# Kernel tuning notes

Hardware: AMD Instinct MI355X
Metric: run time of the kernel (lower is better)

The kernel has to match this reference:

```python
import jax, jax.numpy as jnp
import numpy as np

N, B, L = 1000, 16, 12
H, IN_DIM, OUT_DIM, E = 64, 3, 1, 16000


def _gru_cell(x, h, Wi, Wh, bi, bh):
    # torch nn.GRU gate order: r, z, n
    gi = x @ Wi.T + bi
    gh = h @ Wh.T + bh
    ir, iz, inn = jnp.split(gi, 3, axis=-1)
    hr, hz, hn = jnp.split(gh, 3, axis=-1)
    r = jax.nn.sigmoid(ir + hr)
    z = jax.nn.sigmoid(iz + hz)
    n = jnp.tanh(inn + r * hn)
    return (1.0 - z) * n + z * h


def setup_inputs():
    key = jax.random.key(0)
    ks = jax.random.split(key, 24)
    def rn(k, shape, s=0.1):
        return jax.random.normal(k, shape, dtype=jnp.float32) * s
    return {
        "hidden0": rn(ks[0], (N, B, H), 1.0),
        "hidden1": rn(ks[1], (N, B, H), 1.0),
        "features": rn(ks[2], (N, H), 1.0),
        "labels": rn(ks[3], (N, B, L, IN_DIM), 1.0),
        "edge_index": jax.random.randint(ks[4], (2, E), 0, N),
        # GRU1: input_dim -> H
        "Wi1": rn(ks[5], (3 * H, IN_DIM)), "Wh1": rn(ks[6], (3 * H, H)),
        "bi1": rn(ks[7], (3 * H,)), "bh1": rn(ks[8], (3 * H,)),
        # MetaGAT MLP: 2H -> 16 -> 2 -> 2H*H
        "W1": rn(ks[9], (16, 2 * H)), "b1": rn(ks[10], (16,)),
        "W2": rn(ks[11], (2, 16)), "b2": rn(ks[12], (2,)),
        "W3": rn(ks[13], (2 * H * H, 2)), "b3": rn(ks[14], (2 * H * H,)),
        # GRU2: H -> H
        "Wi2": rn(ks[15], (3 * H, H)), "Wh2": rn(ks[16], (3 * H, H)),
        "bi2": rn(ks[17], (3 * H,)), "bh2": rn(ks[18], (3 * H,)),
        # output layer: 2H -> OUT_DIM
        "Wo": rn(ks[19], (OUT_DIM, 2 * H)), "bo": rn(ks[20], (OUT_DIM,)),
    }


def reference(hidden0, hidden1, features, labels, edge_index,
              Wi1, Wh1, bi1, bh1, W1, b1, W2, b2, W3, b3,
              Wi2, Wh2, bi2, bh2, Wo, bo):
    n, b, length, _ = labels.shape
    h = Wh1.shape[1]
    out_dim = Wo.shape[0]
    in_dim = Wi1.shape[1]
    aux = labels[..., out_dim:]  # [N,B,L,aux_dim]
    # add self loops (as in MetaGAT.forward)
    loops = jnp.arange(n)
    src = jnp.concatenate([edge_index[0], loops])  # j, source
    dst = jnp.concatenate([edge_index[1], loops])  # i, target
    # per-edge weight matrices; features are constant across timesteps so hoist
    ft = jnp.concatenate([features[dst], features[src]], axis=-1)  # [Etot,2H]
    w = jax.nn.sigmoid(ft @ W1.T + b1)
    w = jax.nn.sigmoid(w @ W2.T + b2)
    w = (w @ W3.T + b3).reshape(-1, 2 * h, h)  # [Etot,2H,H]
    feat_b = jnp.broadcast_to(features[:, None, :], (n, b, features.shape[-1]))

    def step(carry, idx):
        h0, h1, prev = carry
        aux_prev = jnp.take(aux, jnp.maximum(idx - 1, 0), axis=2)  # [N,B,aux]
        # eval path (train_mode=False): feed back previous prediction
        data = jnp.where(idx == 0,
                         jnp.zeros((n, b, in_dim), labels.dtype),
                         jnp.concatenate([prev, aux_prev], axis=-1))
        h0n = _gru_cell(data.reshape(n * b, in_dim), h0.reshape(n * b, h),
                        Wi1, Wh1, bi1, bh1).reshape(n, b, h)
        # MetaGAT message passing
        st_j = h0n[src]                                  # [Etot,B,H]
        st = jnp.concatenate([h0n[dst], st_j], axis=-1)  # [Etot,B,2H]
        alpha = jax.nn.leaky_relu(jnp.einsum('ebk,ekh->ebh', st, w), 0.01)
        alpha = jax.nn.softmax(alpha, axis=1)            # softmax over batch dim (faithful to source)
        agg = jax.ops.segment_sum(alpha * st_j, dst, num_segments=n)
        gat = jax.nn.relu(agg)                           # [N,B,H]
        h1n = _gru_cell(gat.reshape(n * b, h), h1.reshape(n * b, h),
                        Wi2, Wh2, bi2, bh2).reshape(n, b, h)
        pred = jnp.concatenate([h1n, feat_b], axis=-1) @ Wo.T + bo  # [N,B,out_dim]
        return (h0n, h1n, pred), pred

    init = (hidden0, hidden1, jnp.zeros((n, b, out_dim), labels.dtype))
    _, preds = jax.lax.scan(step, init, jnp.arange(length))
    return jnp.moveaxis(preds, 0, 2)  # [N,B,L,out_dim]
```

## Files before the change

kernel.cpp:

```cpp
#include <hip/hip_runtime.h>

#define N_NODES 1000
#define BATCH 16
#define SEQ 12
#define IN_DIM 3
#define HDIM 64
#define E_EDGES 16000
#define EN (E_EDGES + N_NODES)
#define NB (N_NODES * BATCH)

typedef unsigned int u32;
typedef unsigned short u16;

__device__ __forceinline__ float sigmoidf(float x) { return 1.0f / (1.0f + expf(-x)); }

__device__ __forceinline__ u16 f2bf(float x) {
    u32 u = __builtin_bit_cast(u32, x);
    u32 r = (u + 0x7fffu + ((u >> 16) & 1u)) >> 16;
    return (u16)r;
}
__device__ __forceinline__ float bf2f(u32 h) {
    return __builtin_bit_cast(float, (h & 0xffffu) << 16);
}
__device__ __forceinline__ u32 pack2(float a, float b) {
    return (u32)f2bf(a) | ((u32)f2bf(b) << 16);
}

__global__ void prep_kernel(const float* __restrict__ hidden0,
                            const float* __restrict__ hidden1,
                            const float* __restrict__ features,
                            const float* __restrict__ W3,
                            const float* __restrict__ b3,
                            const float* __restrict__ Wo,
                            const float* __restrict__ bo,
                            const float* __restrict__ Wh1,
                            const float* __restrict__ Wi1,
                            const float* __restrict__ Wi2,
                            const float* __restrict__ Wh2,
                            float* __restrict__ h0, float* __restrict__ h1,
                            float* __restrict__ M,
                            float* __restrict__ Wh1T, float* __restrict__ Wi1T,
                            float* __restrict__ Wi2T, float* __restrict__ Wh2T,
                            float* __restrict__ fpred, float* __restrict__ prev)
{
    int tid = blockIdx.x * blockDim.x + threadIdx.x;
    int stride = gridDim.x * blockDim.x;

    for (int i = tid; i < NB * HDIM; i += stride) { h0[i] = hidden0[i]; h1[i] = hidden1[i]; }

    for (int i = tid; i < 64 * 384; i += stride) {
        int k = i / 384, c = i % 384;
        int grp = c / 64, h = c % 64;
        int kk = (grp < 3 ? k : 64 + k) * 64 + h;
        float val;
        if (grp == 0 || grp == 3)      val = W3[kk * 2 + 0];
        else if (grp == 1 || grp == 4) val = W3[kk * 2 + 1];
        else                           val = b3[kk];
        M[i] = val;
    }

    for (int i = tid; i < 192 * 64; i += stride) {
        int k = i / 192, gj = i % 192;
        Wh1T[i] = Wh1[gj * 64 + k];
        Wi2T[i] = Wi2[gj * 64 + k];
        Wh2T[i] = Wh2[gj * 64 + k];
    }
    for (int i = tid; i < 3 * 192; i += stride) {
        int c = i / 192, gj = i % 192;
        Wi1T[i] = Wi1[gj * 3 + c];
    }

    for (int i = tid; i < NB; i += stride) prev[i] = 0.0f;

    for (int n = tid; n < N_NODES; n += stride) {
        float acc = bo[0];
        for (int h = 0; h < HDIM; ++h) acc += features[n * HDIM + h] * Wo[64 + h];
        fpred[n] = acc;
    }
}

__global__ void deg_init_kernel(int* __restrict__ deg)
{
    int n = blockIdx.x * blockDim.x + threadIdx.x;
    if (n < N_NODES) deg[n] = 1;
}

__global__ void deg_count_kernel(const int* __restrict__ edge_index, int* __restrict__ deg)
{
    int e = blockIdx.x * blockDim.x + threadIdx.x;
    if (e < E_EDGES) atomicAdd(&deg[edge_index[E_EDGES + e]], 1);
}

__global__ __launch_bounds__(1024) void scan_kernel(const int* __restrict__ deg,
                                                    int* __restrict__ row_ptr,
                                                    int* __restrict__ row_fill)
{
    __shared__ int s[1024];
    int tid = threadIdx.x;
    int x = (tid < N_NODES) ? deg[tid] : 0;
    s[tid] = x;
    __syncthreads();
    for (int off = 1; off < 1024; off <<= 1) {
        int v = (tid >= off) ? s[tid - off] : 0;
        __syncthreads();
        s[tid] += v;
        __syncthreads();
    }
    int incl = s[tid];
    int excl = incl - x;
    if (tid < N_NODES) { row_ptr[tid] = excl; row_fill[tid] = excl; }
    if (tid == N_NODES - 1) row_ptr[N_NODES] = incl;
}

__global__ void scatter_kernel(const int* __restrict__ edge_index,
                               int* __restrict__ row_fill,
                               int* __restrict__ csr_src,
                               int* __restrict__ perm)
{
    int e = blockIdx.x * blockDim.x + threadIdx.x;
    if (e < E_EDGES) {
        int s = edge_index[e];
        int d = edge_index[E_EDGES + e];
        int p = atomicAdd(&row_fill[d], 1);
        csr_src[p] = s;
        perm[e] = p;
    } else if (e < EN) {
        int n = e - E_EDGES;
        int p = atomicAdd(&row_fill[n], 1);
        csr_src[p] = n;
        perm[e] = p;
    }
}

__global__ __launch_bounds__(256) void edge_mlp_kernel(const int* __restrict__ edge_index,
                                                       const float* __restrict__ features,
                                                       const float* __restrict__ W1,
                                                       const float* __restrict__ b1,
                                                       const float* __restrict__ W2,
                                                       const float* __restrict__ b2,
                                                       const int* __restrict__ perm,
                                                       float* __restrict__ csr_uv)
{
    int w = threadIdx.x >> 6, j = threadIdx.x & 63;
    int e = blockIdx.x * 4 + w;
    int s, d;
    if (e < E_EDGES) { s = edge_index[e]; d = edge_index[E_EDGES + e]; }
    else             { s = e - E_EDGES; d = s; }

    __shared__ float ft[4][128];
    __shared__ float w1s[4][16];
    ft[w][j]      = features[d * HDIM + j];
    ft[w][64 + j] = features[s * HDIM + j];
    __syncthreads();

    int o = j & 15, part = j >> 4;
    float acc = 0.0f;
    #pragma unroll 8
    for (int kk = 0; kk < 32; ++kk)
        acc += ft[w][part * 32 + kk] * W1[o * 128 + part * 32 + kk];
    acc += __shfl_xor(acc, 16, 64);
    acc += __shfl_xor(acc, 32, 64);
    if (j < 16) w1s[w][j] = sigmoidf(acc + b1[j]);
    __syncthreads();
    if (j < 2) {
        float a2 = b2[j];
        #pragma unroll
        for (int k = 0; k < 16; ++k) a2 += w1s[w][k] * W2[j * 16 + k];
        csr_uv[perm[e] * 2 + j] = sigmoidf(a2);
    }
}

__global__ __launch_bounds__(256) void gru1_proj_kernel(const float* __restrict__ labels,
                                                        const float* __restrict__ prev,
                                                        const float* __restrict__ Wi1T,
                                                        const float* __restrict__ Wh1T,
                                                        const float* __restrict__ bi1,
                                                        const float* __restrict__ bh1,
                                                        const float* __restrict__ M,
                                                        float* __restrict__ h0,
                                                        uint2* __restrict__ Pd,
                                                        uint2* __restrict__ Ps,
                                                        int t)
{
    int w = threadIdx.x >> 6, j = threadIdx.x & 63;
    int rbase = blockIdx.x * 32 + w * 8;
    __shared__ float hs[32][64];

    #pragma unroll
    for (int rr = 0; rr < 8; ++rr)
        hs[w * 8 + rr][j] = h0[(size_t)(rbase + rr) * HDIM + j];

    float ar[8], az[8], an[8];
    {
        float br = bh1[j], bz = bh1[64 + j], bn = bh1[128 + j];
        #pragma unroll
        for (int rr = 0; rr < 8; ++rr) { ar[rr] = br; az[rr] = bz; an[rr] = bn; }
    }

    for (int k = 0; k < 64; k += 2) {
        const float* w0 = &Wh1T[(size_t)k * 192 + j];
        float wr0 = w0[0], wz0 = w0[64], wn0 = w0[128];
        float wr1 = w0[192], wz1 = w0[256], wn1 = w0[320];
        #pragma unroll
        for (int rr = 0; rr < 8; ++rr) {
            float2 h2 = *(const float2*)&hs[w * 8 + rr][k];
            ar[rr] = fmaf(wr0, h2.x, ar[rr]);
            az[rr] = fmaf(wz0, h2.x, az[rr]);
            an[rr] = fmaf(wn0, h2.x, an[rr]);
            ar[rr] = fmaf(wr1, h2.y, ar[rr]);
            az[rr] = fmaf(wz1, h2.y, az[rr]);
            an[rr] = fmaf(wn1, h2.y, an[rr]);
        }
    }

    float wi00 = Wi1T[j],       wi01 = Wi1T[64 + j],       wi02 = Wi1T[128 + j];
    float wi10 = Wi1T[192 + j], wi11 = Wi1T[192 + 64 + j], wi12 = Wi1T[192 + 128 + j];
    float wi20 = Wi1T[384 + j], wi21 = Wi1T[384 + 64 + j], wi22 = Wi1T[384 + 128 + j];
    float bir = bi1[j], biz = bi1[64 + j], bin_ = bi1[128 + j];

    #pragma unroll
    for (int rr = 0; rr < 8; ++rr) {
        int row = rbase + rr;
        float x0 = 0.f, x1 = 0.f, x2 = 0.f;
        if (t > 0) {
            x0 = prev[row];
            const float* lab = labels + ((size_t)row * SEQ + (t - 1)) * IN_DIM;
            x1 = lab[1]; x2 = lab[2];
        }
        float gir = bir  + x0 * wi00 + x1 * wi10 + x2 * wi20;
        float giz = biz  + x0 * wi01 + x1 * wi11 + x2 * wi21;
        float gin = bin_ + x0 * wi02 + x1 * wi12 + x2 * wi22;
        float rg = sigmoidf(gir + ar[rr]);
        float zg = sigmoidf(giz + az[rr]);
        float ng = tanhf(gin + rg * an[rr]);
        float hj = hs[w * 8 + rr][j];
        float hn = (1.0f - zg) * ng + zg * hj;
        h0[(size_t)row * HDIM + j] = hn;
        hs[w * 8 + rr][j] = hn;
    }

    float a0[8], a1[8], a2[8], a3[8], a4[8], a5[8];
    #pragma unroll
    for (int rr = 0; rr < 8; ++rr) { a0[rr]=0.f; a1[rr]=0.f; a2[rr]=0.f; a3[rr]=0.f; a4[rr]=0.f; a5[rr]=0.f; }

    for (int k = 0; k < 64; ++k) {
        const float* mrow = &M[(size_t)k * 384 + j];
        float m0 = mrow[0],   m1 = mrow[64],  m2 = mrow[128];
        float m3 = mrow[192], m4 = mrow[256], m5 = mrow[320];
        #pragma unroll
        for (int rr = 0; rr < 8; ++rr) {
            float hk = hs[w * 8 + rr][k];
            a0[rr] = fmaf(m0, hk, a0[rr]); a1[rr] = fmaf(m1, hk, a1[rr]);
            a2[rr] = fmaf(m2, hk, a2[rr]); a3[rr] = fmaf(m3, hk, a3[rr]);
            a4[rr] = fmaf(m4, hk, a4[rr]); a5[rr] = fmaf(m5, hk, a5[rr]);
        }
    }

    #pragma unroll
    for (int rr = 0; rr < 8; ++rr) {
        size_t row = rbase + rr;
        float stj = hs[w * 8 + rr][j];
        Pd[row * 64 + j] = make_uint2(pack2(a0[rr], a1[rr]), pack2(a2[rr], 0.f));
        Ps[row * 64 + j] = make_uint2(pack2(a3[rr], a4[rr]), pack2(a5[rr], stj));
    }
}

__global__ __launch_bounds__(256) void edge_step_kernel(const int* __restrict__ row_ptr,
                                                        const int* __restrict__ csr_src,
                                                        const float* __restrict__ csr_uv,
                                                        const uint2* __restrict__ Pd,
                                                        const uint2* __restrict__ Ps,
                                                        float* __restrict__ agg)
{
    int d = blockIdx.x;
    int w = threadIdx.x >> 6, h = threadIdx.x & 63;

    uint2 pdreg[BATCH];
    #pragma unroll
    for (int b = 0; b < BATCH; ++b)
        pdreg[b] = Pd[((size_t)d * BATCH + b) * 64 + h];

    float acc[BATCH];
    #pragma unroll
    for (int b = 0; b < BATCH; ++b) acc[b] = 0.0f;

    int start = row_ptr[d], end = row_ptr[d + 1];
    for (int p = start + w; p < end; p += 4) {
        int s = csr_src[p];
        float u = csr_uv[p * 2], v = csr_uv[p * 2 + 1];

        float al[BATCH], stj[BATCH];
        #pragma unroll
        for (int b = 0; b < BATCH; ++b) {
            uint2 pd = pdreg[b];
            uint2 ps = Ps[((size_t)s * BATCH + b) * 64 + h];
            float c0 = bf2f(pd.x), c1 = bf2f(pd.x >> 16), c2 = bf2f(pd.y);
            float c3 = bf2f(ps.x), c4 = bf2f(ps.x >> 16), c5 = bf2f(ps.y);
            float a = u * (c0 + c3) + v * (c1 + c4) + c2 + c5;
            al[b] = (a > 0.0f) ? a : 0.01f * a;
            stj[b] = bf2f(ps.y >> 16);
        }
        float m = al[0];
        #pragma unroll
        for (int b = 1; b < BATCH; ++b) m = fmaxf(m, al[b]);
        float sum = 0.0f;
        #pragma unroll
        for (int b = 0; b < BATCH; ++b) { al[b] = expf(al[b] - m); sum += al[b]; }
        float inv = 1.0f / sum;
        #pragma unroll
        for (int b = 0; b < BATCH; ++b) acc[b] = fmaf(al[b] * inv, stj[b], acc[b]);
    }

    __shared__ float red[4][BATCH][HDIM];
    #pragma unroll
    for (int b = 0; b < BATCH; ++b) red[w][b][h] = acc[b];
    __syncthreads();

    for (int c = threadIdx.x; c < BATCH * HDIM; c += 256) {
        float s4 = red[0][0][c] + red[1][0][c] + red[2][0][c] + red[3][0][c];
        agg[(size_t)d * BATCH * HDIM + c] = s4;
    }
}

__global__ __launch_bounds__(256) void gru2_pred_kernel(const float* __restrict__ agg,
                                                        const float* __restrict__ Wi2T,
                                                        const float* __restrict__ Wh2T,
                                                        const float* __restrict__ bi2,
                                                        const float* __restrict__ bh2,
                                                        const float* __restrict__ Wo,
                                                        const float* __restrict__ fpred,
                                                        float* __restrict__ h1,
                                                        float* __restrict__ prev,
                                                        float* __restrict__ out,
                                                        int t)
{
    int w = threadIdx.x >> 6, j = threadIdx.x & 63;
    int rbase = blockIdx.x * 32 + w * 8;
    __shared__ float gs[32][64];
    __shared__ float hs[32][64];

    #pragma unroll
    for (int rr = 0; rr < 8; ++rr) {
        float g = agg[(size_t)(rbase + rr) * HDIM + j];
        gs[w * 8 + rr][j] = fmaxf(g, 0.0f);
        hs[w * 8 + rr][j] = h1[(size_t)(rbase + rr) * HDIM + j];
    }

    float acr[8], acz[8], ain[8], ahn[8];
    {
        float b0 = bi2[j] + bh2[j], b1 = bi2[64 + j] + bh2[64 + j];
        float b2 = bi2[128 + j], c2 = bh2[128 + j];
        #pragma unroll
        for (int rr = 0; rr < 8; ++rr) { acr[rr] = b0; acz[rr] = b1; ain[rr] = b2; ahn[rr] = c2; }
    }

    for (int k = 0; k < 64; ++k) {
        const float* wiRow = &Wi2T[(size_t)k * 192 + j];
        const float* whRow = &Wh2T[(size_t)k * 192 + j];
        float wir = wiRow[0], wiz = wiRow[64], win = wiRow[128];
        float whr = whRow[0], whz = whRow[64], whn = whRow[128];
        #pragma unroll
        for (int rr = 0; rr < 8; ++rr) {
            float gk = gs[w * 8 + rr][k];
            float hk = hs[w * 8 + rr][k];
            acr[rr] = fmaf(wir, gk, acr[rr]);  acr[rr] = fmaf(whr, hk, acr[rr]);
            acz[rr] = fmaf(wiz, gk, acz[rr]);  acz[rr] = fmaf(whz, hk, acz[rr]);
            ain[rr] = fmaf(win, gk, ain[rr]);  ahn[rr] = fmaf(whn, hk, ahn[rr]);
        }
    }

    float woj = Wo[j];
    #pragma unroll
    for (int rr = 0; rr < 8; ++rr) {
        float rg = sigmoidf(acr[rr]);
        float zg = sigmoidf(acz[rr]);
        float ng = tanhf(ain[rr] + rg * ahn[rr]);
        float hj = hs[w * 8 + rr][j];
        float hn = (1.0f - zg) * ng + zg * hj;
        h1[(size_t)(rbase + rr) * HDIM + j] = hn;

        float part = hn * woj;
        #pragma unroll
        for (int off = 32; off; off >>= 1) part += __shfl_xor(part, off, 64);
        if (j == rr) {
            int row = rbase + rr;
            float p = part + fpred[row / BATCH];
            prev[row] = p;
            out[(size_t)row * SEQ + t] = p;
        }
    }
}

extern "C" void kernel_launch(void* const* d_in, const int* in_sizes, int n_in,
                              void* d_out, int out_size, void* d_ws, size_t ws_size,
                              hipStream_t stream)
{
    const float* hidden0  = (const float*)d_in[0];
    const float* hidden1  = (const float*)d_in[1];
    const float* features = (const float*)d_in[2];
    const float* labels   = (const float*)d_in[3];
    const int*   edge_idx = (const int*)d_in[4];
    const float* Wi1 = (const float*)d_in[5];
    const float* Wh1 = (const float*)d_in[6];
    const float* bi1 = (const float*)d_in[7];
    const float* bh1 = (const float*)d_in[8];
    const float* W1  = (const float*)d_in[9];
    const float* b1  = (const float*)d_in[10];
    const float* W2  = (const float*)d_in[11];
    const float* b2  = (const float*)d_in[12];
    const float* W3  = (const float*)d_in[13];
    const float* b3  = (const float*)d_in[14];
    const float* Wi2 = (const float*)d_in[15];
    const float* Wh2 = (const float*)d_in[16];
    const float* bi2 = (const float*)d_in[17];
    const float* bh2 = (const float*)d_in[18];
    const float* Wo  = (const float*)d_in[19];
    const float* bo  = (const float*)d_in[20];

    float* ws = (float*)d_ws;
    float* h0    = ws;  ws += NB * HDIM;
    float* h1    = ws;  ws += NB * HDIM;
    uint2* Pd    = (uint2*)ws;  ws += NB * HDIM * 2;
    uint2* Ps    = (uint2*)ws;  ws += NB * HDIM * 2;
    float* agg   = ws;  ws += NB * HDIM;
    float* csr_uv= ws;  ws += EN * 2;
    float* M     = ws;  ws += 64 * 384;
    float* Wh1T  = ws;  ws += 64 * 192;
    float* Wi1T  = ws;  ws += 3 * 192;
    float* Wi2T  = ws;  ws += 64 * 192;
    float* Wh2T  = ws;  ws += 64 * 192;
    float* fpred = ws;  ws += N_NODES;
    float* prev  = ws;  ws += NB;
    int*   deg      = (int*)ws;  ws += N_NODES;
    int*   row_ptr  = (int*)ws;  ws += N_NODES + 1;
    int*   row_fill = (int*)ws;  ws += N_NODES;
    int*   csr_src  = (int*)ws;  ws += EN;
    int*   perm     = (int*)ws;  ws += EN;
    float* out   = (float*)d_out;

    prep_kernel<<<256, 256, 0, stream>>>(hidden0, hidden1, features, W3, b3, Wo, bo,
                                         Wh1, Wi1, Wi2, Wh2,
                                         h0, h1, M, Wh1T, Wi1T, Wi2T, Wh2T, fpred, prev);
    deg_init_kernel<<<(N_NODES + 255) / 256, 256, 0, stream>>>(deg);
    deg_count_kernel<<<(E_EDGES + 255) / 256, 256, 0, stream>>>(edge_idx, deg);
    scan_kernel<<<1, 1024, 0, stream>>>(deg, row_ptr, row_fill);
    scatter_kernel<<<(EN + 255) / 256, 256, 0, stream>>>(edge_idx, row_fill, csr_src, perm);
    edge_mlp_kernel<<<(EN + 3) / 4, 256, 0, stream>>>(edge_idx, features, W1, b1, W2, b2,
                                                      perm, csr_uv);

    for (int t = 0; t < SEQ; ++t) {
        gru1_proj_kernel<<<NB / 32, 256, 0, stream>>>(labels, prev, Wi1T, Wh1T, bi1, bh1,
                                                      M, h0, Pd, Ps, t);
        edge_step_kernel<<<N_NODES, 256, 0, stream>>>(row_ptr, csr_src, csr_uv, Pd, Ps, agg);
        gru2_pred_kernel<<<NB / 32, 256, 0, stream>>>(agg, Wi2T, Wh2T, bi2, bh2, Wo, fpred,
                                                      h1, prev, out, t);
    }
}
```

Measured before the change: 993.9 us.

## Fuse edge aggregation, GRU2, prediction and next-step GRU1 into one per-node kernel

The per-timestep edge aggregation, GRU2 plus output prediction, and the next timestep's GRU1 plus projection are merged into a single kernel with one block per destination node. A separate t=0 GRU1 kernel runs before the loop. Ping-pong Pd/Ps buffers keep the reads of the current projections apart from the writes of the next ones. This drops the agg and prev global round trips and two launches per step, but the per-node blocks now handle only 16 rows each and run the GRU matmuls with 4 rows per wave instead of 8, which lowers weight reuse.

```diff
diff --git a/kernel.cpp b/kernel.cpp
--- a/kernel.cpp
+++ b/kernel.cpp
@@ -41,7 +41,7 @@
                             float* __restrict__ M,
                             float* __restrict__ Wh1T, float* __restrict__ Wi1T,
                             float* __restrict__ Wi2T, float* __restrict__ Wh2T,
-                            float* __restrict__ fpred, float* __restrict__ prev)
+                            float* __restrict__ fpred)
 {
     int tid = blockIdx.x * blockDim.x + threadIdx.x;
     int stride = gridDim.x * blockDim.x;
@@ -69,8 +69,6 @@
         int c = i / 192, gj = i % 192;
         Wi1T[i] = Wi1[gj * 3 + c];
     }
-
-    for (int i = tid; i < NB; i += stride) prev[i] = 0.0f;
 
     for (int n = tid; n < N_NODES; n += stride) {
         float acc = bo[0];
@@ -170,17 +168,13 @@
     }
 }
 
-__global__ __launch_bounds__(256) void gru1_proj_kernel(const float* __restrict__ labels,
-                                                        const float* __restrict__ prev,
-                                                        const float* __restrict__ Wi1T,
-                                                        const float* __restrict__ Wh1T,
-                                                        const float* __restrict__ bi1,
-                                                        const float* __restrict__ bh1,
-                                                        const float* __restrict__ M,
-                                                        float* __restrict__ h0,
-                                                        uint2* __restrict__ Pd,
-                                                        uint2* __restrict__ Ps,
-                                                        int t)
+__global__ __launch_bounds__(256) void gru1_proj_t0_kernel(const float* __restrict__ Wh1T,
+                                                           const float* __restrict__ bi1,
+                                                           const float* __restrict__ bh1,
+                                                           const float* __restrict__ M,
+                                                           float* __restrict__ h0,
+                                                           uint2* __restrict__ Pd,
+                                                           uint2* __restrict__ Ps)
 {
     int w = threadIdx.x >> 6, j = threadIdx.x & 63;
     int rbase = blockIdx.x * 32 + w * 8;
@@ -213,43 +207,238 @@
         }
     }
 
+    float bir = bi1[j], biz = bi1[64 + j], bin_ = bi1[128 + j];
+
+    #pragma unroll
+    for (int rr = 0; rr < 8; ++rr) {
+        float rg = sigmoidf(bir + ar[rr]);
+        float zg = sigmoidf(biz + az[rr]);
+        float ng = tanhf(bin_ + rg * an[rr]);
+        float hj = hs[w * 8 + rr][j];
+        float hn = (1.0f - zg) * ng + zg * hj;
+        h0[(size_t)(rbase + rr) * HDIM + j] = hn;
+        hs[w * 8 + rr][j] = hn;
+    }
+
+    float a0[8], a1[8], a2[8], a3[8], a4[8], a5[8];
+    #pragma unroll
+    for (int rr = 0; rr < 8; ++rr) { a0[rr]=0.f; a1[rr]=0.f; a2[rr]=0.f; a3[rr]=0.f; a4[rr]=0.f; a5[rr]=0.f; }
+
+    for (int k = 0; k < 64; ++k) {
+        const float* mrow = &M[(size_t)k * 384 + j];
+        float m0 = mrow[0],   m1 = mrow[64],  m2 = mrow[128];
+        float m3 = mrow[192], m4 = mrow[256], m5 = mrow[320];
+        #pragma unroll
+        for (int rr = 0; rr < 8; ++rr) {
+            float hk = hs[w * 8 + rr][k];
+            a0[rr] = fmaf(m0, hk, a0[rr]); a1[rr] = fmaf(m1, hk, a1[rr]);
+            a2[rr] = fmaf(m2, hk, a2[rr]); a3[rr] = fmaf(m3, hk, a3[rr]);
+            a4[rr] = fmaf(m4, hk, a4[rr]); a5[rr] = fmaf(m5, hk, a5[rr]);
+        }
+    }
+
+    #pragma unroll
+    for (int rr = 0; rr < 8; ++rr) {
+        size_t row = rbase + rr;
+        float stj = hs[w * 8 + rr][j];
+        Pd[row * 64 + j] = make_uint2(pack2(a0[rr], a1[rr]), pack2(a2[rr], 0.f));
+        Ps[row * 64 + j] = make_uint2(pack2(a3[rr], a4[rr]), pack2(a5[rr], stj));
+    }
+}
+
+__global__ __launch_bounds__(256) void step_kernel(const int* __restrict__ row_ptr,
+                                                   const int* __restrict__ csr_src,
+                                                   const float* __restrict__ csr_uv,
+                                                   const uint2* __restrict__ Pdr,
+                                                   const uint2* __restrict__ Psr,
+                                                   uint2* __restrict__ Pdw,
+                                                   uint2* __restrict__ Psw,
+                                                   const float* __restrict__ Wi2T,
+                                                   const float* __restrict__ Wh2T,
+                                                   const float* __restrict__ bi2,
+                                                   const float* __restrict__ bh2,
+                                                   const float* __restrict__ Wo,
+                                                   const float* __restrict__ fpred,
+                                                   float* __restrict__ h1,
+                                                   float* __restrict__ out,
+                                                   const float* __restrict__ labels,
+                                                   const float* __restrict__ Wi1T,
+                                                   const float* __restrict__ Wh1T,
+                                                   const float* __restrict__ bi1,
+                                                   const float* __restrict__ bh1,
+                                                   const float* __restrict__ M,
+                                                   float* __restrict__ h0,
+                                                   int t, int last)
+{
+    int d = blockIdx.x;
+    int w = threadIdx.x >> 6, j = threadIdx.x & 63;
+    int rbase = d * BATCH + w * 4;
+
+    __shared__ float red[4][BATCH][HDIM];
+    __shared__ float gs[BATCH][HDIM];
+    __shared__ float hs[BATCH][HDIM];
+    __shared__ float prevs[BATCH];
+
+    uint2 pdreg[BATCH];
+    #pragma unroll
+    for (int b = 0; b < BATCH; ++b)
+        pdreg[b] = Pdr[((size_t)d * BATCH + b) * 64 + j];
+
+    float acc[BATCH];
+    #pragma unroll
+    for (int b = 0; b < BATCH; ++b) acc[b] = 0.0f;
+
+    int start = row_ptr[d], end = row_ptr[d + 1];
+    for (int p = start + w; p < end; p += 4) {
+        int s = csr_src[p];
+        float u = csr_uv[p * 2], v = csr_uv[p * 2 + 1];
+
+        float al[BATCH], stj[BATCH];
+        #pragma unroll
+        for (int b = 0; b < BATCH; ++b) {
+            uint2 pd = pdreg[b];
+            uint2 ps = Psr[((size_t)s * BATCH + b) * 64 + j];
+            float a = u * (bf2f(pd.x) + bf2f(ps.x))
+                    + v * (bf2f(pd.x >> 16) + bf2f(ps.x >> 16))
+                    + bf2f(pd.y) + bf2f(ps.y);
+            al[b] = (a > 0.0f) ? a : 0.01f * a;
+            stj[b] = bf2f(ps.y >> 16);
+        }
+        float m = al[0];
+        #pragma unroll
+        for (int b = 1; b < BATCH; ++b) m = fmaxf(m, al[b]);
+        float sum = 0.0f;
+        #pragma unroll
+        for (int b = 0; b < BATCH; ++b) { al[b] = expf(al[b] - m); sum += al[b]; }
+        float inv = 1.0f / sum;
+        #pragma unroll
+        for (int b = 0; b < BATCH; ++b) acc[b] = fmaf(al[b] * inv, stj[b], acc[b]);
+    }
+
+    #pragma unroll
+    for (int b = 0; b < BATCH; ++b) red[w][b][j] = acc[b];
+
+    #pragma unroll
+    for (int rr = 0; rr < 4; ++rr)
+        hs[w * 4 + rr][j] = h1[(size_t)(rbase + rr) * HDIM + j];
+
+    __syncthreads();
+
+    for (int c = threadIdx.x; c < BATCH * HDIM; c += 256) {
+        float s4 = red[0][0][c] + red[1][0][c] + red[2][0][c] + red[3][0][c];
+        gs[0][c] = fmaxf(s4, 0.0f);
+    }
+    __syncthreads();
+
+    float acr[4], acz[4], ain[4], ahn[4];
+    {
+        float b0 = bi2[j] + bh2[j], b1 = bi2[64 + j] + bh2[64 + j];
+        float b2 = bi2[128 + j], c2 = bh2[128 + j];
+        #pragma unroll
+        for (int rr = 0; rr < 4; ++rr) { acr[rr] = b0; acz[rr] = b1; ain[rr] = b2; ahn[rr] = c2; }
+    }
+
+    for (int k = 0; k < 64; ++k) {
+        const float* wiRow = &Wi2T[(size_t)k * 192 + j];
+        const float* whRow = &Wh2T[(size_t)k * 192 + j];
+        float wir = wiRow[0], wiz = wiRow[64], win = wiRow[128];
+        float whr = whRow[0], whz = whRow[64], whn = whRow[128];
+        #pragma unroll
+        for (int rr = 0; rr < 4; ++rr) {
+            float gk = gs[w * 4 + rr][k];
+            float hk = hs[w * 4 + rr][k];
+            acr[rr] = fmaf(wir, gk, acr[rr]);  acr[rr] = fmaf(whr, hk, acr[rr]);
+            acz[rr] = fmaf(wiz, gk, acz[rr]);  acz[rr] = fmaf(whz, hk, acz[rr]);
+            ain[rr] = fmaf(win, gk, ain[rr]);  ahn[rr] = fmaf(whn, hk, ahn[rr]);
+        }
+    }
+
+    float woj = Wo[j];
+    float fp = fpred[d];
+    #pragma unroll
+    for (int rr = 0; rr < 4; ++rr) {
+        float rg = sigmoidf(acr[rr]);
+        float zg = sigmoidf(acz[rr]);
+        float ng = tanhf(ain[rr] + rg * ahn[rr]);
+        float hj = hs[w * 4 + rr][j];
+        float hn = (1.0f - zg) * ng + zg * hj;
+        h1[(size_t)(rbase + rr) * HDIM + j] = hn;
+
+        float part = hn * woj;
+        #pragma unroll
+        for (int off = 32; off; off >>= 1) part += __shfl_xor(part, off, 64);
+        if (j == rr) {
+            float p = part + fp;
+            prevs[w * 4 + rr] = p;
+            out[(size_t)(rbase + rr) * SEQ + t] = p;
+        }
+    }
+    __syncthreads();
+
+    if (last) return;
+
+    #pragma unroll
+    for (int rr = 0; rr < 4; ++rr)
+        gs[w * 4 + rr][j] = h0[(size_t)(rbase + rr) * HDIM + j];
+
+    float ar[4], az[4], an1[4];
+    {
+        float br = bh1[j], bz = bh1[64 + j], bn = bh1[128 + j];
+        #pragma unroll
+        for (int rr = 0; rr < 4; ++rr) { ar[rr] = br; az[rr] = bz; an1[rr] = bn; }
+    }
+
+    for (int k = 0; k < 64; k += 2) {
+        const float* w0 = &Wh1T[(size_t)k * 192 + j];
+        float wr0 = w0[0], wz0 = w0[64], wn0 = w0[128];
+        float wr1 = w0[192], wz1 = w0[256], wn1 = w0[320];
+        #pragma unroll
+        for (int rr = 0; rr < 4; ++rr) {
+            float2 h2 = *(const float2*)&gs[w * 4 + rr][k];
+            ar[rr]  = fmaf(wr0, h2.x, ar[rr]);
+            az[rr]  = fmaf(wz0, h2.x, az[rr]);
+            an1[rr] = fmaf(wn0, h2.x, an1[rr]);
+            ar[rr]  = fmaf(wr1, h2.y, ar[rr]);
+            az[rr]  = fmaf(wz1, h2.y, az[rr]);
+            an1[rr] = fmaf(wn1, h2.y, an1[rr]);
+        }
+    }
+
     float wi00 = Wi1T[j],       wi01 = Wi1T[64 + j],       wi02 = Wi1T[128 + j];
     float wi10 = Wi1T[192 + j], wi11 = Wi1T[192 + 64 + j], wi12 = Wi1T[192 + 128 + j];
     float wi20 = Wi1T[384 + j], wi21 = Wi1T[384 + 64 + j], wi22 = Wi1T[384 + 128 + j];
     float bir = bi1[j], biz = bi1[64 + j], bin_ = bi1[128 + j];
 
     #pragma unroll
-    for (int rr = 0; rr < 8; ++rr) {
+    for (int rr = 0; rr < 4; ++rr) {
         int row = rbase + rr;
-        float x0 = 0.f, x1 = 0.f, x2 = 0.f;
-        if (t > 0) {
-            x0 = prev[row];
-            const float* lab = labels + ((size_t)row * SEQ + (t - 1)) * IN_DIM;
-            x1 = lab[1]; x2 = lab[2];
-        }
+        float x0 = prevs[w * 4 + rr];
+        const float* lab = labels + ((size_t)row * SEQ + t) * IN_DIM;
+        float x1 = lab[1], x2 = lab[2];
+
         float gir = bir  + x0 * wi00 + x1 * wi10 + x2 * wi20;
         float giz = biz  + x0 * wi01 + x1 * wi11 + x2 * wi21;
         float gin = bin_ + x0 * wi02 + x1 * wi12 + x2 * wi22;
         float rg = sigmoidf(gir + ar[rr]);
         float zg = sigmoidf(giz + az[rr]);
-        float ng = tanhf(gin + rg * an[rr]);
-        float hj = hs[w * 8 + rr][j];
+        float ng = tanhf(gin + rg * an1[rr]);
+        float hj = gs[w * 4 + rr][j];
         float hn = (1.0f - zg) * ng + zg * hj;
         h0[(size_t)row * HDIM + j] = hn;
-        hs[w * 8 + rr][j] = hn;
-    }
-
-    float a0[8], a1[8], a2[8], a3[8], a4[8], a5[8];
-    #pragma unroll
-    for (int rr = 0; rr < 8; ++rr) { a0[rr]=0.f; a1[rr]=0.f; a2[rr]=0.f; a3[rr]=0.f; a4[rr]=0.f; a5[rr]=0.f; }
+        gs[w * 4 + rr][j] = hn;
+    }
+
+    float a0[4], a1[4], a2[4], a3[4], a4[4], a5[4];
+    #pragma unroll
+    for (int rr = 0; rr < 4; ++rr) { a0[rr]=0.f; a1[rr]=0.f; a2[rr]=0.f; a3[rr]=0.f; a4[rr]=0.f; a5[rr]=0.f; }
 
     for (int k = 0; k < 64; ++k) {
         const float* mrow = &M[(size_t)k * 384 + j];
         float m0 = mrow[0],   m1 = mrow[64],  m2 = mrow[128];
         float m3 = mrow[192], m4 = mrow[256], m5 = mrow[320];
         #pragma unroll
-        for (int rr = 0; rr < 8; ++rr) {
-            float hk = hs[w * 8 + rr][k];
+        for (int rr = 0; rr < 4; ++rr) {
+            float hk = gs[w * 4 + rr][k];
             a0[rr] = fmaf(m0, hk, a0[rr]); a1[rr] = fmaf(m1, hk, a1[rr]);
             a2[rr] = fmaf(m2, hk, a2[rr]); a3[rr] = fmaf(m3, hk, a3[rr]);
             a4[rr] = fmaf(m4, hk, a4[rr]); a5[rr] = fmaf(m5, hk, a5[rr]);
@@ -257,137 +446,11 @@
     }
 
     #pragma unroll
-    for (int rr = 0; rr < 8; ++rr) {
+    for (int rr = 0; rr < 4; ++rr) {
         size_t row = rbase + rr;
-        float stj = hs[w * 8 + rr][j];
-        Pd[row * 64 + j] = make_uint2(pack2(a0[rr], a1[rr]), pack2(a2[rr], 0.f));
-        Ps[row * 64 + j] = make_uint2(pack2(a3[rr], a4[rr]), pack2(a5[rr], stj));
-    }
-}
-
-__global__ __launch_bounds__(256) void edge_step_kernel(const int* __restrict__ row_ptr,
-                                                        const int* __restrict__ csr_src,
-                                                        const float* __restrict__ csr_uv,
-                                                        const uint2* __restrict__ Pd,
-                                                        const uint2* __restrict__ Ps,
-                                                        float* __restrict__ agg)
-{
-    int d = blockIdx.x;
-    int w = threadIdx.x >> 6, h = threadIdx.x & 63;
-
-    uint2 pdreg[BATCH];
-    #pragma unroll
-    for (int b = 0; b < BATCH; ++b)
-        pdreg[b] = Pd[((size_t)d * BATCH + b) * 64 + h];
-
-    float acc[BATCH];
-    #pragma unroll
-    for (int b = 0; b < BATCH; ++b) acc[b] = 0.0f;
-
-    int start = row_ptr[d], end = row_ptr[d + 1];
-    for (int p = start + w; p < end; p += 4) {
-        int s = csr_src[p];
-        float u = csr_uv[p * 2], v = csr_uv[p * 2 + 1];
-
-        float al[BATCH], stj[BATCH];
-        #pragma unroll
-        for (int b = 0; b < BATCH; ++b) {
-            uint2 pd = pdreg[b];
-            uint2 ps = Ps[((size_t)s * BATCH + b) * 64 + h];
-            float c0 = bf2f(pd.x), c1 = bf2f(pd.x >> 16), c2 = bf2f(pd.y);
-            float c3 = bf2f(ps.x), c4 = bf2f(ps.x >> 16), c5 = bf2f(ps.y);
-            float a = u * (c0 + c3) + v * (c1 + c4) + c2 + c5;
-            al[b] = (a > 0.0f) ? a : 0.01f * a;
-            stj[b] = bf2f(ps.y >> 16);
-        }
-        float m = al[0];
-        #pragma unroll
-        for (int b = 1; b < BATCH; ++b) m = fmaxf(m, al[b]);
-        float sum = 0.0f;
-        #pragma unroll
-        for (int b = 0; b < BATCH; ++b) { al[b] = expf(al[b] - m); sum += al[b]; }
-        float inv = 1.0f / sum;
-        #pragma unroll
-        for (int b = 0; b < BATCH; ++b) acc[b] = fmaf(al[b] * inv, stj[b], acc[b]);
-    }
-
-    __shared__ float red[4][BATCH][HDIM];
-    #pragma unroll
-    for (int b = 0; b < BATCH; ++b) red[w][b][h] = acc[b];
-    __syncthreads();
-
-    for (int c = threadIdx.x; c < BATCH * HDIM; c += 256) {
-        float s4 = red[0][0][c] + red[1][0][c] + red[2][0][c] + red[3][0][c];
-        agg[(size_t)d * BATCH * HDIM + c] = s4;
-    }
-}
-
-__global__ __launch_bounds__(256) void gru2_pred_kernel(const float* __restrict__ agg,
-                                                        const float* __restrict__ Wi2T,
-                                                        const float* __restrict__ Wh2T,
-                                                        const float* __restrict__ bi2,
-                                                        const float* __restrict__ bh2,
-                                                        const float* __restrict__ Wo,
-                                                        const float* __restrict__ fpred,
-                                                        float* __restrict__ h1,
-                                                        float* __restrict__ prev,
-                                                        float* __restrict__ out,
-                                                        int t)
-{
-    int w = threadIdx.x >> 6, j = threadIdx.x & 63;
-    int rbase = blockIdx.x * 32 + w * 8;
-    __shared__ float gs[32][64];
-    __shared__ float hs[32][64];
-
-    #pragma unroll
-    for (int rr = 0; rr < 8; ++rr) {
-        float g = agg[(size_t)(rbase + rr) * HDIM + j];
-        gs[w * 8 + rr][j] = fmaxf(g, 0.0f);
-        hs[w * 8 + rr][j] = h1[(size_t)(rbase + rr) * HDIM + j];
-    }
-
-    float acr[8], acz[8], ain[8], ahn[8];
-    {
-        float b0 = bi2[j] + bh2[j], b1 = bi2[64 + j] + bh2[64 + j];
-        float b2 = bi2[128 + j], c2 = bh2[128 + j];
-        #pragma unroll
-        for (int rr = 0; rr < 8; ++rr) { acr[rr] = b0; acz[rr] = b1; ain[rr] = b2; ahn[rr] = c2; }
-    }
-
-    for (int k = 0; k < 64; ++k) {
-        const float* wiRow = &Wi2T[(size_t)k * 192 + j];
-        const float* whRow = &Wh2T[(size_t)k * 192 + j];
-        float wir = wiRow[0], wiz = wiRow[64], win = wiRow[128];
-        float whr = whRow[0], whz = whRow[64], whn = whRow[128];
-        #pragma unroll
-        for (int rr = 0; rr < 8; ++rr) {
-            float gk = gs[w * 8 + rr][k];
-            float hk = hs[w * 8 + rr][k];
-            acr[rr] = fmaf(wir, gk, acr[rr]);  acr[rr] = fmaf(whr, hk, acr[rr]);
-            acz[rr] = fmaf(wiz, gk, acz[rr]);  acz[rr] = fmaf(whz, hk, acz[rr]);
-            ain[rr] = fmaf(win, gk, ain[rr]);  ahn[rr] = fmaf(whn, hk, ahn[rr]);
-        }
-    }
-
-    float woj = Wo[j];
-    #pragma unroll
-    for (int rr = 0; rr < 8; ++rr) {
-        float rg = sigmoidf(acr[rr]);
-        float zg = sigmoidf(acz[rr]);
-        float ng = tanhf(ain[rr] + rg * ahn[rr]);
-        float hj = hs[w * 8 + rr][j];
-        float hn = (1.0f - zg) * ng + zg * hj;
-        h1[(size_t)(rbase + rr) * HDIM + j] = hn;
-
-        float part = hn * woj;
-        #pragma unroll
-        for (int off = 32; off; off >>= 1) part += __shfl_xor(part, off, 64);
-        if (j == rr) {
-            int row = rbase + rr;
-            float p = part + fpred[row / BATCH];
-            prev[row] = p;
-            out[(size_t)row * SEQ + t] = p;
-        }
+        float stj = gs[w * 4 + rr][j];
+        Pdw[row * 64 + j] = make_uint2(pack2(a0[rr], a1[rr]), pack2(a2[rr], 0.f));
+        Psw[row * 64 + j] = make_uint2(pack2(a3[rr], a4[rr]), pack2(a5[rr], stj));
     }
 }
 
@@ -420,9 +483,11 @@
     float* ws = (float*)d_ws;
     float* h0    = ws;  ws += NB * HDIM;
     float* h1    = ws;  ws += NB * HDIM;
-    uint2* Pd    = (uint2*)ws;  ws += NB * HDIM * 2;
-    uint2* Ps    = (uint2*)ws;  ws += NB * HDIM * 2;
-    float* agg   = ws;  ws += NB * HDIM;
+    uint2* PdBuf[2]; uint2* PsBuf[2];
+    PdBuf[0] = (uint2*)ws;  ws += NB * HDIM * 2;
+    PsBuf[0] = (uint2*)ws;  ws += NB * HDIM * 2;
+    PdBuf[1] = (uint2*)ws;  ws += NB * HDIM * 2;
+    PsBuf[1] = (uint2*)ws;  ws += NB * HDIM * 2;
     float* csr_uv= ws;  ws += EN * 2;
     float* M     = ws;  ws += 64 * 384;
     float* Wh1T  = ws;  ws += 64 * 192;
@@ -430,7 +495,6 @@
     float* Wi2T  = ws;  ws += 64 * 192;
     float* Wh2T  = ws;  ws += 64 * 192;
     float* fpred = ws;  ws += N_NODES;
-    float* prev  = ws;  ws += NB;
     int*   deg      = (int*)ws;  ws += N_NODES;
     int*   row_ptr  = (int*)ws;  ws += N_NODES + 1;
     int*   row_fill = (int*)ws;  ws += N_NODES;
@@ -440,7 +504,7 @@
 
     prep_kernel<<<256, 256, 0, stream>>>(hidden0, hidden1, features, W3, b3, Wo, bo,
                                          Wh1, Wi1, Wi2, Wh2,
-                                         h0, h1, M, Wh1T, Wi1T, Wi2T, Wh2T, fpred, prev);
+                                         h0, h1, M, Wh1T, Wi1T, Wi2T, Wh2T, fpred);
     deg_init_kernel<<<(N_NODES + 255) / 256, 256, 0, stream>>>(deg);
     deg_count_kernel<<<(E_EDGES + 255) / 256, 256, 0, stream>>>(edge_idx, deg);
     scan_kernel<<<1, 1024, 0, stream>>>(deg, row_ptr, row_fill);
@@ -448,11 +512,17 @@
     edge_mlp_kernel<<<(EN + 3) / 4, 256, 0, stream>>>(edge_idx, features, W1, b1, W2, b2,
                                                       perm, csr_uv);
 
+    gru1_proj_t0_kernel<<<NB / 32, 256, 0, stream>>>(Wh1T, bi1, bh1, M, h0,
+                                                     PdBuf[0], PsBuf[0]);
+
     for (int t = 0; t < SEQ; ++t) {
-        gru1_proj_kernel<<<NB / 32, 256, 0, stream>>>(labels, prev, Wi1T, Wh1T, bi1, bh1,
-                                                      M, h0, Pd, Ps, t);
-        edge_step_kernel<<<N_NODES, 256, 0, stream>>>(row_ptr, csr_src, csr_uv, Pd, Ps, agg);
-        gru2_pred_kernel<<<NB / 32, 256, 0, stream>>>(agg, Wi2T, Wh2T, bi2, bh2, Wo, fpred,
-                                                      h1, prev, out, t);
-    }
-}
+        int par = t & 1;
+        step_kernel<<<N_NODES, 256, 0, stream>>>(row_ptr, csr_src, csr_uv,
+                                                 PdBuf[par], PsBuf[par],
+                                                 PdBuf[par ^ 1], PsBuf[par ^ 1],
+                                                 Wi2T, Wh2T, bi2, bh2, Wo, fpred,
+                                                 h1, out,
+                                                 labels, Wi1T, Wh1T, bi1, bh1, M, h0,
+                                                 t, (t == SEQ - 1) ? 1 : 0);
+    }
+}
```

Measured after the change: 1.565 ms. 57.5% more time.

## Stage bf16-packed GRU and projection weights in shared memory with larger blocks

Applied to the files above, without the earlier changes.

Weights for both GRU cells and the edge projection matrix are packed as bf16 pairs in the prep kernel. Each block stages them into LDS, and the inner loops read them from there instead of from global/L2. Blocks double to 512 threads covering 64 rows, to amortise the staging. This lowers weight precision to bf16 and uses much more LDS per block, which can limit occupancy and leaves fewer blocks than CUs.

```diff
diff --git a/kernel.cpp b/kernel.cpp
--- a/kernel.cpp
+++ b/kernel.cpp
@@ -38,39 +38,59 @@
                             const float* __restrict__ Wi2,
                             const float* __restrict__ Wh2,
                             float* __restrict__ h0, float* __restrict__ h1,
-                            float* __restrict__ M,
-                            float* __restrict__ Wh1T, float* __restrict__ Wi1T,
-                            float* __restrict__ Wi2T, float* __restrict__ Wh2T,
-                            float* __restrict__ fpred, float* __restrict__ prev)
+                            u32* __restrict__ WhPair,
+                            u32* __restrict__ Mpair,
+                            u32* __restrict__ W2pair,
+                            float* __restrict__ Wi1T,
+                            float* __restrict__ fpred)
 {
     int tid = blockIdx.x * blockDim.x + threadIdx.x;
     int stride = gridDim.x * blockDim.x;
 
     for (int i = tid; i < NB * HDIM; i += stride) { h0[i] = hidden0[i]; h1[i] = hidden1[i]; }
 
-    for (int i = tid; i < 64 * 384; i += stride) {
-        int k = i / 384, c = i % 384;
-        int grp = c / 64, h = c % 64;
-        int kk = (grp < 3 ? k : 64 + k) * 64 + h;
-        float val;
-        if (grp == 0 || grp == 3)      val = W3[kk * 2 + 0];
-        else if (grp == 1 || grp == 4) val = W3[kk * 2 + 1];
-        else                           val = b3[kk];
-        M[i] = val;
-    }
-
-    for (int i = tid; i < 192 * 64; i += stride) {
-        int k = i / 192, gj = i % 192;
-        Wh1T[i] = Wh1[gj * 64 + k];
-        Wi2T[i] = Wi2[gj * 64 + k];
-        Wh2T[i] = Wh2[gj * 64 + k];
-    }
+    for (int i = tid; i < 32 * 192; i += stride) {
+        int k2 = i / 192, rem = i % 192;
+        int row = rem;
+        WhPair[i] = pack2(Wh1[row * 64 + 2 * k2], Wh1[row * 64 + 2 * k2 + 1]);
+    }
+
+    for (int i = tid; i < 32 * 384; i += stride) {
+        int k2 = i / 384, rem = i % 384;
+        int c = rem / 64, h = rem % 64;
+        int sel = c % 3;
+        float v0, v1;
+        {
+            int k = 2 * k2;
+            int kk = (c < 3 ? k : 64 + k) * 64 + h;
+            v0 = (sel == 0) ? W3[kk * 2] : (sel == 1) ? W3[kk * 2 + 1] : b3[kk];
+        }
+        {
+            int k = 2 * k2 + 1;
+            int kk = (c < 3 ? k : 64 + k) * 64 + h;
+            v1 = (sel == 0) ? W3[kk * 2] : (sel == 1) ? W3[kk * 2 + 1] : b3[kk];
+        }
+        Mpair[i] = pack2(v0, v1);
+    }
+
+    for (int i = tid; i < 32 * 384; i += stride) {
+        int k2 = i / 384, rem = i % 384;
+        int c = rem / 64, j = rem % 64;
+        float v0, v1;
+        if (c < 3) {
+            int row = c * 64 + j;
+            v0 = Wi2[row * 64 + 2 * k2]; v1 = Wi2[row * 64 + 2 * k2 + 1];
+        } else {
+            int row = (c - 3) * 64 + j;
+            v0 = Wh2[row * 64 + 2 * k2]; v1 = Wh2[row * 64 + 2 * k2 + 1];
+        }
+        W2pair[i] = pack2(v0, v1);
+    }
+
     for (int i = tid; i < 3 * 192; i += stride) {
         int c = i / 192, gj = i % 192;
         Wi1T[i] = Wi1[gj * 3 + c];
     }
-
-    for (int i = tid; i < NB; i += stride) prev[i] = 0.0f;
 
     for (int n = tid; n < N_NODES; n += stride) {
         float acc = bo[0];
@@ -170,25 +190,32 @@
     }
 }
 
-__global__ __launch_bounds__(256) void gru1_proj_kernel(const float* __restrict__ labels,
+__global__ __launch_bounds__(512) void gru1_proj_kernel(const float* __restrict__ labels,
                                                         const float* __restrict__ prev,
                                                         const float* __restrict__ Wi1T,
-                                                        const float* __restrict__ Wh1T,
+                                                        const u32* __restrict__ WhPair,
                                                         const float* __restrict__ bi1,
                                                         const float* __restrict__ bh1,
-                                                        const float* __restrict__ M,
+                                                        const u32* __restrict__ Mpair,
                                                         float* __restrict__ h0,
                                                         uint2* __restrict__ Pd,
                                                         uint2* __restrict__ Ps,
                                                         int t)
 {
-    int w = threadIdx.x >> 6, j = threadIdx.x & 63;
-    int rbase = blockIdx.x * 32 + w * 8;
-    __shared__ float hs[32][64];
-
+    int tid = threadIdx.x;
+    int w = tid >> 6, j = tid & 63;
+    int rbase = blockIdx.x * 64 + w * 8;
+
+    __shared__ u32 sWh[32 * 192];
+    __shared__ u32 sM[32 * 384];
+    __shared__ float hs[64][64];
+
+    for (int i = tid; i < 32 * 192; i += 512) sWh[i] = WhPair[i];
+    for (int i = tid; i < 32 * 384; i += 512) sM[i] = Mpair[i];
     #pragma unroll
     for (int rr = 0; rr < 8; ++rr)
         hs[w * 8 + rr][j] = h0[(size_t)(rbase + rr) * HDIM + j];
+    __syncthreads();
 
     float ar[8], az[8], an[8];
     {
@@ -197,19 +224,19 @@
         for (int rr = 0; rr < 8; ++rr) { ar[rr] = br; az[rr] = bz; an[rr] = bn; }
     }
 
-    for (int k = 0; k < 64; k += 2) {
-        const float* w0 = &Wh1T[(size_t)k * 192 + j];
-        float wr0 = w0[0], wz0 = w0[64], wn0 = w0[128];
-        float wr1 = w0[192], wz1 = w0[256], wn1 = w0[320];
+    for (int k2 = 0; k2 < 32; ++k2) {
+        u32 pr = sWh[k2 * 192 + j];
+        u32 pz = sWh[k2 * 192 + 64 + j];
+        u32 pn = sWh[k2 * 192 + 128 + j];
+        float wr0 = bf2f(pr), wr1 = bf2f(pr >> 16);
+        float wz0 = bf2f(pz), wz1 = bf2f(pz >> 16);
+        float wn0 = bf2f(pn), wn1 = bf2f(pn >> 16);
         #pragma unroll
         for (int rr = 0; rr < 8; ++rr) {
-            float2 h2 = *(const float2*)&hs[w * 8 + rr][k];
-            ar[rr] = fmaf(wr0, h2.x, ar[rr]);
-            az[rr] = fmaf(wz0, h2.x, az[rr]);
-            an[rr] = fmaf(wn0, h2.x, an[rr]);
-            ar[rr] = fmaf(wr1, h2.y, ar[rr]);
-            az[rr] = fmaf(wz1, h2.y, az[rr]);
-            an[rr] = fmaf(wn1, h2.y, an[rr]);
+            float2 h2 = *(const float2*)&hs[w * 8 + rr][2 * k2];
+            ar[rr] = fmaf(wr0, h2.x, ar[rr]); ar[rr] = fmaf(wr1, h2.y, ar[rr]);
+            az[rr] = fmaf(wz0, h2.x, az[rr]); az[rr] = fmaf(wz1, h2.y, az[rr]);
+            an[rr] = fmaf(wn0, h2.x, an[rr]); an[rr] = fmaf(wn1, h2.y, an[rr]);
         }
     }
 
@@ -243,16 +270,28 @@
     #pragma unroll
     for (int rr = 0; rr < 8; ++rr) { a0[rr]=0.f; a1[rr]=0.f; a2[rr]=0.f; a3[rr]=0.f; a4[rr]=0.f; a5[rr]=0.f; }
 
-    for (int k = 0; k < 64; ++k) {
-        const float* mrow = &M[(size_t)k * 384 + j];
-        float m0 = mrow[0],   m1 = mrow[64],  m2 = mrow[128];
-        float m3 = mrow[192], m4 = mrow[256], m5 = mrow[320];
+    for (int k2 = 0; k2 < 32; ++k2) {
+        u32 p0 = sM[k2 * 384 + j];
+        u32 p1 = sM[k2 * 384 + 64 + j];
+        u32 p2 = sM[k2 * 384 + 128 + j];
+        u32 p3 = sM[k2 * 384 + 192 + j];
+        u32 p4 = sM[k2 * 384 + 256 + j];
+        u32 p5 = sM[k2 * 384 + 320 + j];
+        float m00 = bf2f(p0), m01 = bf2f(p0 >> 16);
+        float m10 = bf2f(p1), m11 = bf2f(p1 >> 16);
+        float m20 = bf2f(p2), m21 = bf2f(p2 >> 16);
+        float m30 = bf2f(p3), m31 = bf2f(p3 >> 16);
+        float m40 = bf2f(p4), m41 = bf2f(p4 >> 16);
+        float m50 = bf2f(p5), m51 = bf2f(p5 >> 16);
         #pragma unroll
         for (int rr = 0; rr < 8; ++rr) {
-            float hk = hs[w * 8 + rr][k];
-            a0[rr] = fmaf(m0, hk, a0[rr]); a1[rr] = fmaf(m1, hk, a1[rr]);
-            a2[rr] = fmaf(m2, hk, a2[rr]); a3[rr] = fmaf(m3, hk, a3[rr]);
-            a4[rr] = fmaf(m4, hk, a4[rr]); a5[rr] = fmaf(m5, hk, a5[rr]);
+            float2 h2 = *(const float2*)&hs[w * 8 + rr][2 * k2];
+            a0[rr] = fmaf(m00, h2.x, a0[rr]); a0[rr] = fmaf(m01, h2.y, a0[rr]);
+            a1[rr] = fmaf(m10, h2.x, a1[rr]); a1[rr] = fmaf(m11, h2.y, a1[rr]);
+            a2[rr] = fmaf(m20, h2.x, a2[rr]); a2[rr] = fmaf(m21, h2.y, a2[rr]);
+            a3[rr] = fmaf(m30, h2.x, a3[rr]); a3[rr] = fmaf(m31, h2.y, a3[rr]);
+            a4[rr] = fmaf(m40, h2.x, a4[rr]); a4[rr] = fmaf(m41, h2.y, a4[rr]);
+            a5[rr] = fmaf(m50, h2.x, a5[rr]); a5[rr] = fmaf(m51, h2.y, a5[rr]);
         }
     }
 
@@ -294,9 +333,9 @@
         for (int b = 0; b < BATCH; ++b) {
             uint2 pd = pdreg[b];
             uint2 ps = Ps[((size_t)s * BATCH + b) * 64 + h];
-            float c0 = bf2f(pd.x), c1 = bf2f(pd.x >> 16), c2 = bf2f(pd.y);
-            float c3 = bf2f(ps.x), c4 = bf2f(ps.x >> 16), c5 = bf2f(ps.y);
-            float a = u * (c0 + c3) + v * (c1 + c4) + c2 + c5;
+            float a = u * (bf2f(pd.x) + bf2f(ps.x))
+                    + v * (bf2f(pd.x >> 16) + bf2f(ps.x >> 16))
+                    + bf2f(pd.y) + bf2f(ps.y);
             al[b] = (a > 0.0f) ? a : 0.01f * a;
             stj[b] = bf2f(ps.y >> 16);
         }
@@ -322,9 +361,8 @@
     }
 }
 
-__global__ __launch_bounds__(256) void gru2_pred_kernel(const float* __restrict__ agg,
-                                                        const float* __restrict__ Wi2T,
-                                                        const float* __restrict__ Wh2T,
+__global__ __launch_bounds__(512) void gru2_pred_kernel(const float* __restrict__ agg,
+                                                        const u32* __restrict__ W2pair,
                                                         const float* __restrict__ bi2,
                                                         const float* __restrict__ bh2,
                                                         const float* __restrict__ Wo,
@@ -334,17 +372,22 @@
                                                         float* __restrict__ out,
                                                         int t)
 {
-    int w = threadIdx.x >> 6, j = threadIdx.x & 63;
-    int rbase = blockIdx.x * 32 + w * 8;
-    __shared__ float gs[32][64];
-    __shared__ float hs[32][64];
-
+    int tid = threadIdx.x;
+    int w = tid >> 6, j = tid & 63;
+    int rbase = blockIdx.x * 64 + w * 8;
+
+    __shared__ u32 sW2[32 * 384];
+    __shared__ float gs[64][64];
+    __shared__ float hs[64][64];
+
+    for (int i = tid; i < 32 * 384; i += 512) sW2[i] = W2pair[i];
     #pragma unroll
     for (int rr = 0; rr < 8; ++rr) {
         float g = agg[(size_t)(rbase + rr) * HDIM + j];
         gs[w * 8 + rr][j] = fmaxf(g, 0.0f);
         hs[w * 8 + rr][j] = h1[(size_t)(rbase + rr) * HDIM + j];
     }
+    __syncthreads();
 
     float acr[8], acz[8], ain[8], ahn[8];
     {
@@ -354,18 +397,29 @@
         for (int rr = 0; rr < 8; ++rr) { acr[rr] = b0; acz[rr] = b1; ain[rr] = b2; ahn[rr] = c2; }
     }
 
-    for (int k = 0; k < 64; ++k) {
-        const float* wiRow = &Wi2T[(size_t)k * 192 + j];
-        const float* whRow = &Wh2T[(size_t)k * 192 + j];
-        float wir = wiRow[0], wiz = wiRow[64], win = wiRow[128];
-        float whr = whRow[0], whz = whRow[64], whn = whRow[128];
+    for (int k2 = 0; k2 < 32; ++k2) {
+        u32 pir = sW2[k2 * 384 + j];
+        u32 piz = sW2[k2 * 384 + 64 + j];
+        u32 pin = sW2[k2 * 384 + 128 + j];
+        u32 phr = sW2[k2 * 384 + 192 + j];
+        u32 phz = sW2[k2 * 384 + 256 + j];
+        u32 phn = sW2[k2 * 384 + 320 + j];
+        float wir0 = bf2f(pir), wir1 = bf2f(pir >> 16);
+        float wiz0 = bf2f(piz), wiz1 = bf2f(piz >> 16);
+        float win0 = bf2f(pin), win1 = bf2f(pin >> 16);
+        float whr0 = bf2f(phr), whr1 = bf2f(phr >> 16);
+        float whz0 = bf2f(phz), whz1 = bf2f(phz >> 16);
+        float whn0 = bf2f(phn), whn1 = bf2f(phn >> 16);
         #pragma unroll
         for (int rr = 0; rr < 8; ++rr) {
-            float gk = gs[w * 8 + rr][k];
-            float hk = hs[w * 8 + rr][k];
-            acr[rr] = fmaf(wir, gk, acr[rr]);  acr[rr] = fmaf(whr, hk, acr[rr]);
-            acz[rr] = fmaf(wiz, gk, acz[rr]);  acz[rr] = fmaf(whz, hk, acz[rr]);
-            ain[rr] = fmaf(win, gk, ain[rr]);  ahn[rr] = fmaf(whn, hk, ahn[rr]);
+            float2 g2 = *(const float2*)&gs[w * 8 + rr][2 * k2];
+            float2 h2 = *(const float2*)&hs[w * 8 + rr][2 * k2];
+            acr[rr] = fmaf(wir0, g2.x, acr[rr]); acr[rr] = fmaf(wir1, g2.y, acr[rr]);
+            acr[rr] = fmaf(whr0, h2.x, acr[rr]); acr[rr] = fmaf(whr1, h2.y, acr[rr]);
+            acz[rr] = fmaf(wiz0, g2.x, acz[rr]); acz[rr] = fmaf(wiz1, g2.y, acz[rr]);
+            acz[rr] = fmaf(whz0, h2.x, acz[rr]); acz[rr] = fmaf(whz1, h2.y, acz[rr]);
+            ain[rr] = fmaf(win0, g2.x, ain[rr]); ain[rr] = fmaf(win1, g2.y, ain[rr]);
+            ahn[rr] = fmaf(whn0, h2.x, ahn[rr]); ahn[rr] = fmaf(whn1, h2.y, ahn[rr]);
         }
     }
 
@@ -424,11 +478,10 @@
     uint2* Ps    = (uint2*)ws;  ws += NB * HDIM * 2;
     float* agg   = ws;  ws += NB * HDIM;
     float* csr_uv= ws;  ws += EN * 2;
-    float* M     = ws;  ws += 64 * 384;
-    float* Wh1T  = ws;  ws += 64 * 192;
+    u32*   WhPair = (u32*)ws;  ws += 32 * 192;
+    u32*   Mpair  = (u32*)ws;  ws += 32 * 384;
+    u32*   W2pair = (u32*)ws;  ws += 32 * 384;
     float* Wi1T  = ws;  ws += 3 * 192;
-    float* Wi2T  = ws;  ws += 64 * 192;
-    float* Wh2T  = ws;  ws += 64 * 192;
     float* fpred = ws;  ws += N_NODES;
     float* prev  = ws;  ws += NB;
     int*   deg      = (int*)ws;  ws += N_NODES;
@@ -440,7 +493,7 @@
 
     prep_kernel<<<256, 256, 0, stream>>>(hidden0, hidden1, features, W3, b3, Wo, bo,
                                          Wh1, Wi1, Wi2, Wh2,
-                                         h0, h1, M, Wh1T, Wi1T, Wi2T, Wh2T, fpred, prev);
+                                         h0, h1, WhPair, Mpair, W2pair, Wi1T, fpred);
     deg_init_kernel<<<(N_NODES + 255) / 256, 256, 0, stream>>>(deg);
     deg_count_kernel<<<(E_EDGES + 255) / 256, 256, 0, stream>>>(edge_idx, deg);
     scan_kernel<<<1, 1024, 0, stream>>>(deg, row_ptr, row_fill);
@@ -449,10 +502,10 @@
                                                       perm, csr_uv);
 
     for (int t = 0; t < SEQ; ++t) {
-        gru1_proj_kernel<<<NB / 32, 256, 0, stream>>>(labels, prev, Wi1T, Wh1T, bi1, bh1,
-                                                      M, h0, Pd, Ps, t);
+        gru1_proj_kernel<<<NB / 64, 512, 0, stream>>>(labels, prev, Wi1T, WhPair, bi1, bh1,
+                                                      Mpair, h0, Pd, Ps, t);
         edge_step_kernel<<<N_NODES, 256, 0, stream>>>(row_ptr, csr_src, csr_uv, Pd, Ps, agg);
-        gru2_pred_kernel<<<NB / 32, 256, 0, stream>>>(agg, Wi2T, Wh2T, bi2, bh2, Wo, fpred,
+        gru2_pred_kernel<<<NB / 64, 512, 0, stream>>>(agg, W2pair, bi2, bh2, Wo, fpred,
                                                       h1, prev, out, t);
     }
 }
```

Result: slower. 1.045 ms (+5.2%).
